# Kernel optimization log

Hardware: AMD Instinct MI355X
Metric: run time of the kernel (lower is better)

## Reference

```python
import jax, jax.numpy as jnp
import numpy as np

CONTEXT_SIZE = 256  # hardcoded in source; scale = context_size**-0.5, not head_size
EMBED_DIM = 384
HEAD_SIZE = 64
BATCH = 512
SEQ = 256


def setup_inputs() -> dict:
    key = jax.random.key(0)
    ks = jax.random.split(key, 7)
    s = 1.0 / np.sqrt(EMBED_DIM)
    return {
        "x": jax.random.normal(ks[0], (BATCH, SEQ, EMBED_DIM), jnp.float32),
        "Wq": jax.random.uniform(ks[1], (EMBED_DIM, HEAD_SIZE), jnp.float32, -s, s),
        "bq": jax.random.uniform(ks[2], (HEAD_SIZE,), jnp.float32, -s, s),
        "Wk": jax.random.uniform(ks[3], (EMBED_DIM, HEAD_SIZE), jnp.float32, -s, s),
        "bk": jax.random.uniform(ks[4], (HEAD_SIZE,), jnp.float32, -s, s),
        "Wv": jax.random.uniform(ks[5], (EMBED_DIM, HEAD_SIZE), jnp.float32, -s, s),
        "bv": jax.random.uniform(ks[6], (HEAD_SIZE,), jnp.float32, -s, s),
    }


def reference(x, Wq, bq, Wk, bk, Wv, bv):
    # x: [B, T, D]
    T = x.shape[1]
    q = x @ Wq + bq          # [B, T, H]
    k = x @ Wk + bk          # [B, T, H]
    v = x @ Wv + bv          # [B, T, H]
    scale = CONTEXT_SIZE ** (-0.5)  # faithful: source scales by context_size, not head_size
    scores = jnp.einsum("bth,bsh->bts", q, k) * scale  # [B, T, T]
    causal = jnp.tril(jnp.ones((T, T), dtype=bool))
    scores = jnp.where(causal, scores, -jnp.inf)
    attn = jax.nn.softmax(scores, axis=-1)
    # dropout omitted (eval mode / deterministic reference)
    return jnp.einsum("bts,bsh->bth", attn, v)  # [B, T, H]
```

## Files before the change

kernel.cpp:

```cpp
#include <hip/hip_runtime.h>
#include <hip/hip_bf16.h>
#include <stdint.h>

#define B_ 512
#define T_ 256
#define D_ 384
#define H_ 64

typedef __attribute__((ext_vector_type(8))) short bf16x8;
typedef __attribute__((ext_vector_type(4))) float f32x4;
typedef __attribute__((ext_vector_type(16))) float f32x16;

__device__ __forceinline__ unsigned short f2bf(float f) {
  union { float f; unsigned int u; } a; a.f = f;
  unsigned int r = (a.u + 0x7FFFu + ((a.u >> 16) & 1u)) >> 16;
  return (unsigned short)r;
}

__device__ __forceinline__ unsigned int pkbf(float lo, float hi) {
  unsigned int r;
  asm("v_cvt_pk_bf16_f32 %0, %1, %2" : "=v"(r) : "v"(lo), "v"(hi));
  return r;
}

__global__ void prep_wt(const float* __restrict__ Wq, const float* __restrict__ Wk,
                        const float* __restrict__ Wv, unsigned short* __restrict__ wt) {
  int idx = blockIdx.x * 256 + threadIdx.x;
  if (idx >= 192 * 384) return;
  int k = idx / 192, n = idx - k * 192;
  int sel = n >> 6, c = n & 63;
  const float* W = (sel == 0) ? Wq : ((sel == 1) ? Wk : Wv);
  wt[n * 384 + k] = f2bf(W[k * 64 + c]);
}

__global__ __launch_bounds__(1024) void attn_fused(
    const float* __restrict__ x, const float* __restrict__ bq,
    const float* __restrict__ bk, const float* __restrict__ bv,
    const unsigned short* __restrict__ wt, float* __restrict__ out) {
  extern __shared__ char smem[];
  const int tid = threadIdx.x;
  const int b = blockIdx.x;
  const int wv = tid >> 6, lane = tid & 63;
  const int lo4 = lane & 15, hi4 = lane >> 4;
  const int lo5 = lane & 31, hi5 = lane >> 5;

  const float* xb = x + (size_t)b * T_ * D_;
  const int row0 = 16 * wv + lo4;

  f32x4 acc[12];
#pragma unroll
  for (int ct = 0; ct < 12; ++ct) acc[ct] = (f32x4)0.0f;

  float4 xsA[2], xsB[2];
  {
    const float* p = xb + row0 * D_ + 8 * hi4;
    xsA[0] = *reinterpret_cast<const float4*>(p);
    xsA[1] = *reinterpret_cast<const float4*>(p + 4);
  }

#pragma unroll
  for (int i = 0; i < 9; ++i) {
    int u = tid + 1024 * i;
    int n = u / 48;
    int mp = u - n * 48;
    int m = (mp & ~7) | ((mp & 7) ^ (n & 7));
    const uint4* src = reinterpret_cast<const uint4*>(wt + n * 384 + 8 * m);
    *reinterpret_cast<uint4*>(smem + 16 * u) = *src;
  }
  __syncthreads();

#pragma unroll
  for (int g = 0; g < 12; ++g) {
    float4* cur = ((g & 1) == 0) ? xsA : xsB;
    float4* nxt = ((g & 1) == 0) ? xsB : xsA;
    if (g < 11) {
      const float* p = xb + row0 * D_ + 32 * (g + 1) + 8 * hi4;
      nxt[0] = *reinterpret_cast<const float4*>(p);
      nxt[1] = *reinterpret_cast<const float4*>(p + 4);
    }
    union { bf16x8 v; unsigned int w[4]; } A;
    A.w[0] = pkbf(cur[0].x, cur[0].y); A.w[1] = pkbf(cur[0].z, cur[0].w);
    A.w[2] = pkbf(cur[1].x, cur[1].y); A.w[3] = pkbf(cur[1].z, cur[1].w);
    bf16x8 afr = A.v;
#pragma unroll
    for (int ct = 0; ct < 12; ++ct) {
      int n = 16 * ct + lo4;
      int kbyte = (64 * g + 16 * hi4) ^ ((n & 7) << 4);
      bf16x8 bw = *reinterpret_cast<const bf16x8*>(smem + n * 768 + kbyte);
      acc[ct] = __builtin_amdgcn_mfma_f32_16x16x32_bf16(afr, bw, acc[ct], 0, 0, 0);
    }
  }
  __syncthreads();

#pragma unroll
  for (int ct = 0; ct < 12; ++ct) {
    int n = 16 * ct + lo4;
    float bias = (ct < 4) ? bq[n] : ((ct < 8) ? bk[n - 64] : bv[n - 128]);
    int rowb = 16 * wv + 4 * hi4;
#pragma unroll
    for (int r = 0; r < 4; ++r) {
      int row = rowb + r;
      unsigned short v = f2bf(acc[ct][r] + bias);
      if (ct < 4) {
        int h = n;
        *reinterpret_cast<unsigned short*>(smem + row * 128 + ((2 * h) ^ ((row & 7) << 4))) = v;
      } else if (ct < 8) {
        int h = n - 64;
        *reinterpret_cast<unsigned short*>(smem + 32768 + row * 128 + ((2 * h) ^ ((row & 7) << 4))) = v;
      } else {
        int h = n - 128;
        *reinterpret_cast<unsigned short*>(smem + 65536 + h * 512 + ((2 * row) ^ ((h & 7) << 4))) = v;
      }
    }
  }
  __syncthreads();

  if (wv < 8) {
    const float cexp = 0.09016844005555897f;

    bf16x8 qf[4];
    {
      int row = 32 * wv + lo5;
#pragma unroll
      for (int s = 0; s < 4; ++s)
        qf[s] = *reinterpret_cast<const bf16x8*>(
            smem + row * 128 + (((32 * s + 16 * hi5)) ^ ((row & 7) << 4)));
    }

    f32x16 o0 = (f32x16)0.0f, o1 = (f32x16)0.0f;
    float lsum = 0.0f;

    for (int kb = 0; kb <= wv; ++kb) {
      f32x16 st = (f32x16)0.0f;
      {
        int row = 32 * kb + lo5;
#pragma unroll
        for (int s = 0; s < 4; ++s) {
          bf16x8 kf = *reinterpret_cast<const bf16x8*>(
              smem + 32768 + row * 128 + (((32 * s + 16 * hi5)) ^ ((row & 7) << 4)));
          st = __builtin_amdgcn_mfma_f32_32x32x16_bf16(kf, qf[s], st, 0, 0, 0);
        }
      }
      float p[16];
#pragma unroll
      for (int r = 0; r < 16; ++r) {
        float e = exp2f(cexp * st[r]);
        if (kb == wv) {
          int keyl = (r & 3) + 8 * (r >> 2) + 4 * hi5;
          if (keyl > lo5) e = 0.0f;
        }
        p[r] = e;
        lsum += e;
      }

      union { bf16x8 v; unsigned int w[4]; } A0, A1;
      {
        unsigned int X0 = pkbf(p[0], p[1]),  X1 = pkbf(p[2], p[3]);
        unsigned int Y0 = pkbf(p[4], p[5]),  Y1 = pkbf(p[6], p[7]);
        unsigned int X0p = (unsigned int)__shfl_xor((int)X0, 32);
        unsigned int X1p = (unsigned int)__shfl_xor((int)X1, 32);
        unsigned int Y0p = (unsigned int)__shfl_xor((int)Y0, 32);
        unsigned int Y1p = (unsigned int)__shfl_xor((int)Y1, 32);
        A0.w[0] = hi5 ? Y0p : X0;
        A0.w[1] = hi5 ? Y1p : X1;
        A0.w[2] = hi5 ? Y0  : X0p;
        A0.w[3] = hi5 ? Y1  : X1p;
        unsigned int Z0 = pkbf(p[8], p[9]),   Z1 = pkbf(p[10], p[11]);
        unsigned int W0 = pkbf(p[12], p[13]), W1 = pkbf(p[14], p[15]);
        unsigned int Z0p = (unsigned int)__shfl_xor((int)Z0, 32);
        unsigned int Z1p = (unsigned int)__shfl_xor((int)Z1, 32);
        unsigned int W0p = (unsigned int)__shfl_xor((int)W0, 32);
        unsigned int W1p = (unsigned int)__shfl_xor((int)W1, 32);
        A1.w[0] = hi5 ? W0p : Z0;
        A1.w[1] = hi5 ? W1p : Z1;
        A1.w[2] = hi5 ? W0  : Z0p;
        A1.w[3] = hi5 ? W1  : Z1p;
      }
#pragma unroll
      for (int s2 = 0; s2 < 2; ++s2) {
        bf16x8 pa = s2 ? A1.v : A0.v;
        int kk = 32 * kb + 16 * s2 + 8 * hi5;
#pragma unroll
        for (int ht = 0; ht < 2; ++ht) {
          int h = 32 * ht + lo5;
          bf16x8 vf = *reinterpret_cast<const bf16x8*>(
              smem + 65536 + h * 512 + (((2 * kk)) ^ ((h & 7) << 4)));
          if (ht == 0) o0 = __builtin_amdgcn_mfma_f32_32x32x16_bf16(pa, vf, o0, 0, 0, 0);
          else         o1 = __builtin_amdgcn_mfma_f32_32x32x16_bf16(pa, vf, o1, 0, 0, 0);
        }
      }
    }

    lsum += __shfl_xor(lsum, 32);
    float inv = 1.0f / lsum;
    float* ob = out + (size_t)b * T_ * H_;
#pragma unroll
    for (int r = 0; r < 16; ++r) {
      int ridx = (r & 3) + 8 * (r >> 2) + 4 * hi5;
      float invr = __shfl(inv, ridx);
      int row = 32 * wv + ridx;
      ob[row * H_ + lo5]      = o0[r] * invr;
      ob[row * H_ + 32 + lo5] = o1[r] * invr;
    }
  }
}

extern "C" void kernel_launch(void* const* d_in, const int* in_sizes, int n_in,
                              void* d_out, int out_size, void* d_ws, size_t ws_size,
                              hipStream_t stream) {
  const float* x  = (const float*)d_in[0];
  const float* Wq = (const float*)d_in[1];
  const float* bq = (const float*)d_in[2];
  const float* Wk = (const float*)d_in[3];
  const float* bk = (const float*)d_in[4];
  const float* Wv = (const float*)d_in[5];
  const float* bv = (const float*)d_in[6];
  unsigned short* wt = (unsigned short*)d_ws;
  float* out = (float*)d_out;

  prep_wt<<<288, 256, 0, stream>>>(Wq, Wk, Wv, wt);
  attn_fused<<<B_, 1024, 147456, stream>>>(x, bq, bk, bv, wt, out);
}
```

Before: 62.35 us.

## Shrink LDS footprint by staging weights in k-slices and splitting K/V halves

Weight tiles are streamed through LDS in six 64-wide k slices instead of loading the full transposed weight matrix. K and V are materialized in two 128-row halves, and attention runs in two phases around a barrier. This cuts dynamic shared memory from 144KB to 64KB so two blocks can share a CU and overlap latency. It adds extra barriers per block, and waves 8-15 sit idle during the first attention phase.

```diff
diff --git a/kernel.cpp b/kernel.cpp
--- a/kernel.cpp
+++ b/kernel.cpp
@@ -6,6 +6,9 @@
 #define T_ 256
 #define D_ 384
 #define H_ 64
+
+#define KK_ 32768
+#define VT_ 49152
 
 typedef __attribute__((ext_vector_type(8))) short bf16x8;
 typedef __attribute__((ext_vector_type(4))) float f32x4;
@@ -43,6 +46,7 @@
   const int wv = tid >> 6, lane = tid & 63;
   const int lo4 = lane & 15, hi4 = lane >> 4;
   const int lo5 = lane & 31, hi5 = lane >> 5;
+  const int qq = wv & 7;
 
   const float* xb = x + (size_t)b * T_ * D_;
   const int row0 = 16 * wv + lo4;
@@ -58,137 +62,190 @@
     xsA[1] = *reinterpret_cast<const float4*>(p + 4);
   }
 
-#pragma unroll
-  for (int i = 0; i < 9; ++i) {
-    int u = tid + 1024 * i;
-    int n = u / 48;
-    int mp = u - n * 48;
-    int m = (mp & ~7) | ((mp & 7) ^ (n & 7));
-    const uint4* src = reinterpret_cast<const uint4*>(wt + n * 384 + 8 * m);
-    *reinterpret_cast<uint4*>(smem + 16 * u) = *src;
-  }
-  __syncthreads();
-
-#pragma unroll
-  for (int g = 0; g < 12; ++g) {
-    float4* cur = ((g & 1) == 0) ? xsA : xsB;
-    float4* nxt = ((g & 1) == 0) ? xsB : xsA;
-    if (g < 11) {
-      const float* p = xb + row0 * D_ + 32 * (g + 1) + 8 * hi4;
-      nxt[0] = *reinterpret_cast<const float4*>(p);
-      nxt[1] = *reinterpret_cast<const float4*>(p + 4);
-    }
-    union { bf16x8 v; unsigned int w[4]; } A;
-    A.w[0] = pkbf(cur[0].x, cur[0].y); A.w[1] = pkbf(cur[0].z, cur[0].w);
-    A.w[2] = pkbf(cur[1].x, cur[1].y); A.w[3] = pkbf(cur[1].z, cur[1].w);
-    bf16x8 afr = A.v;
-#pragma unroll
-    for (int ct = 0; ct < 12; ++ct) {
-      int n = 16 * ct + lo4;
-      int kbyte = (64 * g + 16 * hi4) ^ ((n & 7) << 4);
-      bf16x8 bw = *reinterpret_cast<const bf16x8*>(smem + n * 768 + kbyte);
-      acc[ct] = __builtin_amdgcn_mfma_f32_16x16x32_bf16(afr, bw, acc[ct], 0, 0, 0);
-    }
-  }
-  __syncthreads();
-
-#pragma unroll
-  for (int ct = 0; ct < 12; ++ct) {
+  for (int s = 0; s < 6; ++s) {
+    if (s > 0) __syncthreads();
+#pragma unroll
+    for (int i = 0; i < 2; ++i) {
+      int u = tid + 1024 * i;
+      if (u < 1536) {
+        int n = u >> 3;
+        int mp = u & 7;
+        int m = mp ^ (n & 7);
+        uint4 v = *reinterpret_cast<const uint4*>(wt + n * 384 + 64 * s + 8 * m);
+        *reinterpret_cast<uint4*>(smem + 16 * u) = v;
+      }
+    }
+    __syncthreads();
+#pragma unroll
+    for (int sub = 0; sub < 2; ++sub) {
+      int g = 2 * s + sub;
+      float4* cur = ((g & 1) == 0) ? xsA : xsB;
+      float4* nxt = ((g & 1) == 0) ? xsB : xsA;
+      if (g < 11) {
+        const float* p = xb + row0 * D_ + 32 * (g + 1) + 8 * hi4;
+        nxt[0] = *reinterpret_cast<const float4*>(p);
+        nxt[1] = *reinterpret_cast<const float4*>(p + 4);
+      }
+      union { bf16x8 v; unsigned int w[4]; } A;
+      A.w[0] = pkbf(cur[0].x, cur[0].y); A.w[1] = pkbf(cur[0].z, cur[0].w);
+      A.w[2] = pkbf(cur[1].x, cur[1].y); A.w[3] = pkbf(cur[1].z, cur[1].w);
+      bf16x8 afr = A.v;
+#pragma unroll
+      for (int ct = 0; ct < 12; ++ct) {
+        int n = 16 * ct + lo4;
+        int kbyte = (64 * sub + 16 * hi4) ^ ((n & 7) << 4);
+        bf16x8 bw = *reinterpret_cast<const bf16x8*>(smem + n * 128 + kbyte);
+        acc[ct] = __builtin_amdgcn_mfma_f32_16x16x32_bf16(afr, bw, acc[ct], 0, 0, 0);
+      }
+    }
+  }
+  __syncthreads();
+
+#pragma unroll
+  for (int ct = 0; ct < 4; ++ct) {
     int n = 16 * ct + lo4;
-    float bias = (ct < 4) ? bq[n] : ((ct < 8) ? bk[n - 64] : bv[n - 128]);
+    float bias = bq[n];
     int rowb = 16 * wv + 4 * hi4;
 #pragma unroll
     for (int r = 0; r < 4; ++r) {
       int row = rowb + r;
-      unsigned short v = f2bf(acc[ct][r] + bias);
-      if (ct < 4) {
-        int h = n;
-        *reinterpret_cast<unsigned short*>(smem + row * 128 + ((2 * h) ^ ((row & 7) << 4))) = v;
-      } else if (ct < 8) {
-        int h = n - 64;
-        *reinterpret_cast<unsigned short*>(smem + 32768 + row * 128 + ((2 * h) ^ ((row & 7) << 4))) = v;
-      } else {
-        int h = n - 128;
-        *reinterpret_cast<unsigned short*>(smem + 65536 + h * 512 + ((2 * row) ^ ((h & 7) << 4))) = v;
-      }
-    }
+      *reinterpret_cast<unsigned short*>(
+          smem + row * 128 + ((2 * n) ^ ((row & 7) << 4))) = f2bf(acc[ct][r] + bias);
+    }
+  }
+  __syncthreads();
+
+  bf16x8 qf[4];
+  {
+    int row = 32 * qq + lo5;
+#pragma unroll
+    for (int s = 0; s < 4; ++s)
+      qf[s] = *reinterpret_cast<const bf16x8*>(
+          smem + row * 128 + (((32 * s + 16 * hi5)) ^ ((row & 7) << 4)));
   }
   __syncthreads();
 
   if (wv < 8) {
-    const float cexp = 0.09016844005555897f;
-
-    bf16x8 qf[4];
+#pragma unroll
+    for (int ct = 4; ct < 12; ++ct) {
+      int n = 16 * ct + lo4;
+      float bias = (ct < 8) ? bk[n - 64] : bv[n - 128];
+      int rowb = 16 * wv + 4 * hi4;
+#pragma unroll
+      for (int r = 0; r < 4; ++r) {
+        int row = rowb + r;
+        unsigned short v = f2bf(acc[ct][r] + bias);
+        if (ct < 8) {
+          int h = n - 64;
+          *reinterpret_cast<unsigned short*>(
+              smem + KK_ + row * 128 + ((2 * h) ^ ((row & 7) << 4))) = v;
+        } else {
+          int h = n - 128;
+          *reinterpret_cast<unsigned short*>(
+              smem + VT_ + h * 256 + ((2 * row) ^ ((h & 7) << 4))) = v;
+        }
+      }
+    }
+  }
+  __syncthreads();
+
+  const float cexp = 0.09016844005555897f;
+  f32x16 o0 = (f32x16)0.0f, o1 = (f32x16)0.0f;
+  float lsum = 0.0f;
+
+  auto tile = [&](int klocal, bool diag) {
+    f32x16 st = (f32x16)0.0f;
     {
-      int row = 32 * wv + lo5;
-#pragma unroll
-      for (int s = 0; s < 4; ++s)
-        qf[s] = *reinterpret_cast<const bf16x8*>(
-            smem + row * 128 + (((32 * s + 16 * hi5)) ^ ((row & 7) << 4)));
-    }
-
-    f32x16 o0 = (f32x16)0.0f, o1 = (f32x16)0.0f;
-    float lsum = 0.0f;
-
-    for (int kb = 0; kb <= wv; ++kb) {
-      f32x16 st = (f32x16)0.0f;
-      {
-        int row = 32 * kb + lo5;
-#pragma unroll
-        for (int s = 0; s < 4; ++s) {
-          bf16x8 kf = *reinterpret_cast<const bf16x8*>(
-              smem + 32768 + row * 128 + (((32 * s + 16 * hi5)) ^ ((row & 7) << 4)));
-          st = __builtin_amdgcn_mfma_f32_32x32x16_bf16(kf, qf[s], st, 0, 0, 0);
+      int row = 32 * klocal + lo5;
+#pragma unroll
+      for (int s = 0; s < 4; ++s) {
+        bf16x8 kf = *reinterpret_cast<const bf16x8*>(
+            smem + KK_ + row * 128 + (((32 * s + 16 * hi5)) ^ ((row & 7) << 4)));
+        st = __builtin_amdgcn_mfma_f32_32x32x16_bf16(kf, qf[s], st, 0, 0, 0);
+      }
+    }
+    float p[16];
+#pragma unroll
+    for (int r = 0; r < 16; ++r) {
+      float e = exp2f(cexp * st[r]);
+      if (diag) {
+        int keyl = (r & 3) + 8 * (r >> 2) + 4 * hi5;
+        if (keyl > lo5) e = 0.0f;
+      }
+      p[r] = e;
+      lsum += e;
+    }
+    union { bf16x8 v; unsigned int w[4]; } A0, A1;
+    {
+      unsigned int X0 = pkbf(p[0], p[1]),  X1 = pkbf(p[2], p[3]);
+      unsigned int Y0 = pkbf(p[4], p[5]),  Y1 = pkbf(p[6], p[7]);
+      unsigned int X0p = (unsigned int)__shfl_xor((int)X0, 32);
+      unsigned int X1p = (unsigned int)__shfl_xor((int)X1, 32);
+      unsigned int Y0p = (unsigned int)__shfl_xor((int)Y0, 32);
+      unsigned int Y1p = (unsigned int)__shfl_xor((int)Y1, 32);
+      A0.w[0] = hi5 ? Y0p : X0;
+      A0.w[1] = hi5 ? Y1p : X1;
+      A0.w[2] = hi5 ? Y0  : X0p;
+      A0.w[3] = hi5 ? Y1  : X1p;
+      unsigned int Z0 = pkbf(p[8], p[9]),   Z1 = pkbf(p[10], p[11]);
+      unsigned int W0 = pkbf(p[12], p[13]), W1 = pkbf(p[14], p[15]);
+      unsigned int Z0p = (unsigned int)__shfl_xor((int)Z0, 32);
+      unsigned int Z1p = (unsigned int)__shfl_xor((int)Z1, 32);
+      unsigned int W0p = (unsigned int)__shfl_xor((int)W0, 32);
+      unsigned int W1p = (unsigned int)__shfl_xor((int)W1, 32);
+      A1.w[0] = hi5 ? W0p : Z0;
+      A1.w[1] = hi5 ? W1p : Z1;
+      A1.w[2] = hi5 ? W0  : Z0p;
+      A1.w[3] = hi5 ? W1  : Z1p;
+    }
+#pragma unroll
+    for (int s2 = 0; s2 < 2; ++s2) {
+      bf16x8 pa = s2 ? A1.v : A0.v;
+      int kk = 32 * klocal + 16 * s2 + 8 * hi5;
+#pragma unroll
+      for (int ht = 0; ht < 2; ++ht) {
+        int h = 32 * ht + lo5;
+        bf16x8 vf = *reinterpret_cast<const bf16x8*>(
+            smem + VT_ + h * 256 + (((2 * kk)) ^ ((h & 7) << 4)));
+        if (ht == 0) o0 = __builtin_amdgcn_mfma_f32_32x32x16_bf16(pa, vf, o0, 0, 0, 0);
+        else         o1 = __builtin_amdgcn_mfma_f32_32x32x16_bf16(pa, vf, o1, 0, 0, 0);
+      }
+    }
+  };
+
+  if (wv < 8) {
+    int kbmax = (qq < 4) ? qq : 3;
+    for (int kb = 0; kb <= kbmax; ++kb) tile(kb, kb == qq);
+  }
+  __syncthreads();
+
+  if (wv >= 8) {
+#pragma unroll
+    for (int ct = 4; ct < 12; ++ct) {
+      int n = 16 * ct + lo4;
+      float bias = (ct < 8) ? bk[n - 64] : bv[n - 128];
+      int rowb = 16 * wv + 4 * hi4;
+#pragma unroll
+      for (int r = 0; r < 4; ++r) {
+        int rowl = rowb + r - 128;
+        unsigned short v = f2bf(acc[ct][r] + bias);
+        if (ct < 8) {
+          int h = n - 64;
+          *reinterpret_cast<unsigned short*>(
+              smem + KK_ + rowl * 128 + ((2 * h) ^ ((rowl & 7) << 4))) = v;
+        } else {
+          int h = n - 128;
+          *reinterpret_cast<unsigned short*>(
+              smem + VT_ + h * 256 + ((2 * rowl) ^ ((h & 7) << 4))) = v;
         }
       }
-      float p[16];
-#pragma unroll
-      for (int r = 0; r < 16; ++r) {
-        float e = exp2f(cexp * st[r]);
-        if (kb == wv) {
-          int keyl = (r & 3) + 8 * (r >> 2) + 4 * hi5;
-          if (keyl > lo5) e = 0.0f;
-        }
-        p[r] = e;
-        lsum += e;
-      }
-
-      union { bf16x8 v; unsigned int w[4]; } A0, A1;
-      {
-        unsigned int X0 = pkbf(p[0], p[1]),  X1 = pkbf(p[2], p[3]);
-        unsigned int Y0 = pkbf(p[4], p[5]),  Y1 = pkbf(p[6], p[7]);
-        unsigned int X0p = (unsigned int)__shfl_xor((int)X0, 32);
-        unsigned int X1p = (unsigned int)__shfl_xor((int)X1, 32);
-        unsigned int Y0p = (unsigned int)__shfl_xor((int)Y0, 32);
-        unsigned int Y1p = (unsigned int)__shfl_xor((int)Y1, 32);
-        A0.w[0] = hi5 ? Y0p : X0;
-        A0.w[1] = hi5 ? Y1p : X1;
-        A0.w[2] = hi5 ? Y0  : X0p;
-        A0.w[3] = hi5 ? Y1  : X1p;
-        unsigned int Z0 = pkbf(p[8], p[9]),   Z1 = pkbf(p[10], p[11]);
-        unsigned int W0 = pkbf(p[12], p[13]), W1 = pkbf(p[14], p[15]);
-        unsigned int Z0p = (unsigned int)__shfl_xor((int)Z0, 32);
-        unsigned int Z1p = (unsigned int)__shfl_xor((int)Z1, 32);
-        unsigned int W0p = (unsigned int)__shfl_xor((int)W0, 32);
-        unsigned int W1p = (unsigned int)__shfl_xor((int)W1, 32);
-        A1.w[0] = hi5 ? W0p : Z0;
-        A1.w[1] = hi5 ? W1p : Z1;
-        A1.w[2] = hi5 ? W0  : Z0p;
-        A1.w[3] = hi5 ? W1  : Z1p;
-      }
-#pragma unroll
-      for (int s2 = 0; s2 < 2; ++s2) {
-        bf16x8 pa = s2 ? A1.v : A0.v;
-        int kk = 32 * kb + 16 * s2 + 8 * hi5;
-#pragma unroll
-        for (int ht = 0; ht < 2; ++ht) {
-          int h = 32 * ht + lo5;
-          bf16x8 vf = *reinterpret_cast<const bf16x8*>(
-              smem + 65536 + h * 512 + (((2 * kk)) ^ ((h & 7) << 4)));
-          if (ht == 0) o0 = __builtin_amdgcn_mfma_f32_32x32x16_bf16(pa, vf, o0, 0, 0, 0);
-          else         o1 = __builtin_amdgcn_mfma_f32_32x32x16_bf16(pa, vf, o1, 0, 0, 0);
-        }
-      }
+    }
+  }
+  __syncthreads();
+
+  if (wv < 8) {
+    if (qq >= 4) {
+      for (int kb = 4; kb <= qq; ++kb) tile(kb - 4, kb == qq);
     }
 
     lsum += __shfl_xor(lsum, 32);
@@ -198,7 +255,7 @@
     for (int r = 0; r < 16; ++r) {
       int ridx = (r & 3) + 8 * (r >> 2) + 4 * hi5;
       float invr = __shfl(inv, ridx);
-      int row = 32 * wv + ridx;
+      int row = 32 * qq + ridx;
       ob[row * H_ + lo5]      = o0[r] * invr;
       ob[row * H_ + 32 + lo5] = o1[r] * invr;
     }
@@ -219,5 +276,5 @@
   float* out = (float*)d_out;
 
   prep_wt<<<288, 256, 0, stream>>>(Wq, Wk, Wv, wt);
-  attn_fused<<<B_, 1024, 147456, stream>>>(x, bq, bk, bv, wt, out);
-}
+  attn_fused<<<B_, 1024, 65536, stream>>>(x, bq, bk, bv, wt, out);
+}
```

After: 72.57 us. +16.4%, slower.
